# Performance work log

Hardware: AMD Instinct MI355X
Metric: run time of the kernel (lower is better)

Reference implementation:

```python
import jax, jax.numpy as jnp
import numpy as np

EMBED_DIM = 768
HIDDEN_DIM = 768
ASPECT_NUM = 32
BATCH = 256


def setup_inputs() -> dict:
    key = jax.random.key(0)
    k1, k2, k3, k4, k5, k6, k7 = jax.random.split(key, 7)
    s = 0.02
    return {
        "v_X": jax.random.normal(k1, (BATCH, EMBED_DIM), dtype=jnp.float32),
        "v_H": jax.random.normal(k2, (BATCH, HIDDEN_DIM), dtype=jnp.float32),
        "aspect_ids": jax.random.randint(k3, (BATCH,), 0, ASPECT_NUM, dtype=jnp.int64),
        "W1_embs": s * jax.random.normal(k4, (ASPECT_NUM, (EMBED_DIM + HIDDEN_DIM) * HIDDEN_DIM), dtype=jnp.float32),
        "b1_embs": s * jax.random.normal(k5, (ASPECT_NUM, HIDDEN_DIM), dtype=jnp.float32),
        "W2_embs": s * jax.random.normal(k6, (ASPECT_NUM, HIDDEN_DIM * 2), dtype=jnp.float32),
        "b2_embs": s * jax.random.normal(k7, (ASPECT_NUM, 2), dtype=jnp.float32),
    }


def reference(v_X, v_H, aspect_ids, W1_embs, b1_embs, W2_embs, b2_embs):
    batch = v_X.shape[0]
    V = jnp.concatenate([v_X, v_H], axis=-1)  # (B, E+H)
    W1 = W1_embs[aspect_ids].reshape(batch, EMBED_DIM + HIDDEN_DIM, HIDDEN_DIM)
    b1 = b1_embs[aspect_ids]                  # (B, H)
    W2 = W2_embs[aspect_ids].reshape(batch, HIDDEN_DIM, 2)
    b2 = b2_embs[aspect_ids]                  # (B, 2)
    out1 = jax.nn.relu(jnp.einsum('bd,bdh->bh', V, W1) + b1)  # per-sample GEMV
    logits = jnp.einsum('bh,bht->bt', out1, W2) + b2
    return logits
```

## Files before the change

### kernel.cpp

```cpp
#include <hip/hip_runtime.h>
#include <hip/hip_bf16.h>

#define EMBED 768
#define HID 768
#define DTOT 1536
#define NASP 32
#define BATCHN 256
#define CH 16
#define MAXCHUNK 48
#define COLS 32
#define NT2 (HID / COLS)
#define SROWS 192
#define NSTAGE (DTOT / SROWS)
#define VSP 20


__global__ __launch_bounds__(256, 4) void gemv_fused_kernel(
    const float* __restrict__ vX, const float* __restrict__ vH,
    const float* __restrict__ W1, const int* __restrict__ aspect_ids,
    const float* __restrict__ b1, const float* __restrict__ W2,
    float* __restrict__ plog)
{
    __shared__ int wcnt[4][NASP];
    __shared__ int basearr[NASP];
    __shared__ int countsarr[NASP];
    __shared__ int chasp[MAXCHUNK];
    __shared__ int smpall[MAXCHUNK][CH];
    __shared__ int nchunks_s;
    __shared__ __align__(16) float Vs[SROWS * VSP];
    __shared__ __align__(16) float4 redw[8][4][8];

    int t = threadIdx.x;
    int lane = t & 63;
    int wave = t >> 6;
    int myaid = aspect_ids[t];

    unsigned long long mymask = 0ull;
    for (int a = 0; a < NASP; ++a) {
        bool p = (myaid == a);
        unsigned long long m = __ballot(p);
        if (p) mymask = m;
        if (lane == a) wcnt[wave][a] = __popcll(m);
    }
    __syncthreads();
    if (t < NASP) {
        int ctot = wcnt[0][t] + wcnt[1][t] + wcnt[2][t] + wcnt[3][t];
        countsarr[t] = ctot;
        int nc = (ctot + CH - 1) / CH;
        int incl = nc;
        #pragma unroll
        for (int off = 1; off < NASP; off <<= 1) {
            int v = __shfl_up(incl, off, 64);
            if (t >= off) incl += v;
        }
        int base = incl - nc;
        basearr[t] = base;
        for (int j = 0; j < nc; ++j) chasp[base + j] = t;
        if (t == NASP - 1) nchunks_s = incl;
    }
    __syncthreads();
    {
        int pre = 0;
        for (int w = 0; w < wave; ++w) pre += wcnt[w][myaid];
        int r = pre + __popcll(mymask & ((1ull << lane) - 1ull));
        int c = basearr[myaid] + r / CH;
        smpall[c][r % CH] = t;
    }
    __syncthreads();

    int bid = blockIdx.x;
    int chunk = bid / NT2;
    if (chunk >= nchunks_s) return;
    int tile = bid % NT2;

    int aspect = chasp[chunk];
    int cnt = countsarr[aspect] - CH * (chunk - basearr[aspect]);
    if (cnt > CH) cnt = CH;

    int c8 = t & 7;
    int dg = t >> 3;

    const float* wp = W1 + (size_t)aspect * ((size_t)DTOT * HID)
                         + (size_t)dg * HID + tile * COLS + c8 * 4;

    float4 acc[CH];
    #pragma unroll
    for (int s = 0; s < CH; ++s) { acc[s].x = acc[s].y = acc[s].z = acc[s].w = 0.f; }

    for (int st = 0; st < NSTAGE; ++st) {
        int dbase = st * SROWS;
        __syncthreads();
        #pragma unroll
        for (int r = 0; r < 3; ++r) {
            int id = t + r * 256;
            int s = id & (CH - 1);
            int f = id >> 4;
            int smp = (s < cnt) ? smpall[chunk][s] : smpall[chunk][0];
            int d = dbase + f * 4;
            const float* src = (dbase < EMBED)
                ? (vX + (size_t)smp * EMBED + d)
                : (vH + (size_t)smp * HID + (d - EMBED));
            float4 v = *(const float4*)src;
            Vs[(f * 4 + 0) * VSP + s] = v.x;
            Vs[(f * 4 + 1) * VSP + s] = v.y;
            Vs[(f * 4 + 2) * VSP + s] = v.z;
            Vs[(f * 4 + 3) * VSP + s] = v.w;
        }
        __syncthreads();

        #pragma unroll
        for (int kk = 0; kk < SROWS / 32; ++kk) {
            float4 w = *(const float4*)wp;
            wp += 32 * HID;
            const float* vrow = &Vs[(kk * 32 + dg) * VSP];
            float4 va = *(const float4*)(vrow + 0);
            float4 vb = *(const float4*)(vrow + 4);
            float4 vc = *(const float4*)(vrow + 8);
            float4 vd = *(const float4*)(vrow + 12);
            acc[0].x  += va.x * w.x; acc[0].y  += va.x * w.y; acc[0].z  += va.x * w.z; acc[0].w  += va.x * w.w;
            acc[1].x  += va.y * w.x; acc[1].y  += va.y * w.y; acc[1].z  += va.y * w.z; acc[1].w  += va.y * w.w;
            acc[2].x  += va.z * w.x; acc[2].y  += va.z * w.y; acc[2].z  += va.z * w.z; acc[2].w  += va.z * w.w;
            acc[3].x  += va.w * w.x; acc[3].y  += va.w * w.y; acc[3].z  += va.w * w.z; acc[3].w  += va.w * w.w;
            acc[4].x  += vb.x * w.x; acc[4].y  += vb.x * w.y; acc[4].z  += vb.x * w.z; acc[4].w  += vb.x * w.w;
            acc[5].x  += vb.y * w.x; acc[5].y  += vb.y * w.y; acc[5].z  += vb.y * w.z; acc[5].w  += vb.y * w.w;
            acc[6].x  += vb.z * w.x; acc[6].y  += vb.z * w.y; acc[6].z  += vb.z * w.z; acc[6].w  += vb.z * w.w;
            acc[7].x  += vb.w * w.x; acc[7].y  += vb.w * w.y; acc[7].z  += vb.w * w.z; acc[7].w  += vb.w * w.w;
            acc[8].x  += vc.x * w.x; acc[8].y  += vc.x * w.y; acc[8].z  += vc.x * w.z; acc[8].w  += vc.x * w.w;
            acc[9].x  += vc.y * w.x; acc[9].y  += vc.y * w.y; acc[9].z  += vc.y * w.z; acc[9].w  += vc.y * w.w;
            acc[10].x += vc.z * w.x; acc[10].y += vc.z * w.y; acc[10].z += vc.z * w.z; acc[10].w += vc.z * w.w;
            acc[11].x += vc.w * w.x; acc[11].y += vc.w * w.y; acc[11].z += vc.w * w.z; acc[11].w += vc.w * w.w;
            acc[12].x += vd.x * w.x; acc[12].y += vd.x * w.y; acc[12].z += vd.x * w.z; acc[12].w += vd.x * w.w;
            acc[13].x += vd.y * w.x; acc[13].y += vd.y * w.y; acc[13].z += vd.y * w.z; acc[13].w += vd.y * w.w;
            acc[14].x += vd.z * w.x; acc[14].y += vd.z * w.y; acc[14].z += vd.z * w.z; acc[14].w += vd.z * w.w;
            acc[15].x += vd.w * w.x; acc[15].y += vd.w * w.y; acc[15].z += vd.w * w.z; acc[15].w += vd.w * w.w;
        }
    }

    #pragma unroll
    for (int s = 0; s < CH; ++s) {
        float4 v = acc[s];
        v.x += __shfl_down(v.x, 32, 64); v.y += __shfl_down(v.y, 32, 64);
        v.z += __shfl_down(v.z, 32, 64); v.w += __shfl_down(v.w, 32, 64);
        v.x += __shfl_down(v.x, 16, 64); v.y += __shfl_down(v.y, 16, 64);
        v.z += __shfl_down(v.z, 16, 64); v.w += __shfl_down(v.w, 16, 64);
        v.x += __shfl_down(v.x,  8, 64); v.y += __shfl_down(v.y,  8, 64);
        v.z += __shfl_down(v.z,  8, 64); v.w += __shfl_down(v.w,  8, 64);
        acc[s] = v;
    }

    const float* b1p = b1 + (size_t)aspect * HID;
    const float* w2p = W2 + (size_t)aspect * HID * 2;
    #pragma unroll
    for (int rr = 0; rr < 2; ++rr) {
        __syncthreads();
        if (lane < 8) {
            #pragma unroll
            for (int j = 0; j < 8; ++j)
                redw[j][wave][lane] = acc[rr * 8 + j];
        }
        __syncthreads();
        if (wave == 0) {
            int j = t >> 3;
            int c = t & 7;
            int s = rr * 8 + j;
            float4 a0 = redw[j][0][c], a1 = redw[j][1][c];
            float4 a2 = redw[j][2][c], a3 = redw[j][3][c];
            float4 sum;
            sum.x = a0.x + a1.x + a2.x + a3.x;
            sum.y = a0.y + a1.y + a2.y + a3.y;
            sum.z = a0.z + a1.z + a2.z + a3.z;
            sum.w = a0.w + a1.w + a2.w + a3.w;
            int h = tile * COLS + c * 4;
            float p0 = 0.f, p1 = 0.f;
            if (s < cnt) {
                float o;
                o = fmaxf(sum.x + b1p[h + 0], 0.f); p0 += o * w2p[(h + 0) * 2]; p1 += o * w2p[(h + 0) * 2 + 1];
                o = fmaxf(sum.y + b1p[h + 1], 0.f); p0 += o * w2p[(h + 1) * 2]; p1 += o * w2p[(h + 1) * 2 + 1];
                o = fmaxf(sum.z + b1p[h + 2], 0.f); p0 += o * w2p[(h + 2) * 2]; p1 += o * w2p[(h + 2) * 2 + 1];
                o = fmaxf(sum.w + b1p[h + 3], 0.f); p0 += o * w2p[(h + 3) * 2]; p1 += o * w2p[(h + 3) * 2 + 1];
            }
            p0 += __shfl_down(p0, 4, 64); p1 += __shfl_down(p1, 4, 64);
            p0 += __shfl_down(p0, 2, 64); p1 += __shfl_down(p1, 2, 64);
            p0 += __shfl_down(p0, 1, 64); p1 += __shfl_down(p1, 1, 64);
            if (c == 0 && s < cnt) {
                int smp = smpall[chunk][s];
                float2 pv; pv.x = p0; pv.y = p1;
                *(float2*)&plog[((size_t)tile * BATCHN + smp) * 2] = pv;
            }
        }
    }
}

__global__ __launch_bounds__(BATCHN) void combine_kernel(
    const float* __restrict__ plog, const int* __restrict__ aspect_ids,
    const float* __restrict__ b2, float* __restrict__ logits)
{
    int smp = threadIdx.x;
    int a = aspect_ids[smp];
    float p0 = b2[a * 2 + 0], p1 = b2[a * 2 + 1];
    const float2* pl = (const float2*)plog;
    #pragma unroll
    for (int tl = 0; tl < NT2; ++tl) {
        float2 v = pl[(size_t)tl * BATCHN + smp];
        p0 += v.x; p1 += v.y;
    }
    float2 out; out.x = p0; out.y = p1;
    *(float2*)&logits[smp * 2] = out;
}

extern "C" void kernel_launch(void* const* d_in, const int* in_sizes, int n_in,
                              void* d_out, int out_size, void* d_ws, size_t ws_size,
                              hipStream_t stream) {
    const float* vX  = (const float*)d_in[0];
    const float* vH  = (const float*)d_in[1];
    const int*   aid = (const int*)d_in[2];
    const float* W1  = (const float*)d_in[3];
    const float* b1  = (const float*)d_in[4];
    const float* W2  = (const float*)d_in[5];
    const float* b2  = (const float*)d_in[6];
    float* logits = (float*)d_out;

    float* plog = (float*)d_ws;

    gemv_fused_kernel<<<MAXCHUNK * NT2, 256, 0, stream>>>(
        vX, vH, W1, aid, b1, W2, plog);
    combine_kernel<<<1, BATCHN, 0, stream>>>(plog, aid, b2, logits);
}
```

Measured before the change: 48.58 us.

## Widen column tile to 128 and use 512-thread blocks for grouped GEMV

Each block now covers 128 output columns instead of 32 and runs 512 threads, with 32 threads spanning columns and 16 row groups. The gathered V chunk is loaded into shared memory once per 128 columns instead of once per 32, so V traffic and shared-memory staging per block drop. The grid shrinks from 48*24 to 48*6 blocks. The cross-wave reduction now spans 8 waves and needs more rounds. The bigger blocks and fewer of them may lower occupancy and parallelism, and the setup code now places __syncthreads inside divergent branches.

```diff
diff --git a/kernel.cpp b/kernel.cpp
--- a/kernel.cpp
+++ b/kernel.cpp
@@ -8,14 +8,15 @@
 #define BATCHN 256
 #define CH 16
 #define MAXCHUNK 48
-#define COLS 32
-#define NT2 (HID / COLS)
+#define COLS 128
+#define NT (HID / COLS)
 #define SROWS 192
 #define NSTAGE (DTOT / SROWS)
+#define DG 16
 #define VSP 20
 
 
-__global__ __launch_bounds__(256, 4) void gemv_fused_kernel(
+__global__ __launch_bounds__(512, 2) void gemv_fused_kernel(
     const float* __restrict__ vX, const float* __restrict__ vH,
     const float* __restrict__ W1, const int* __restrict__ aspect_ids,
     const float* __restrict__ b1, const float* __restrict__ W2,
@@ -28,60 +29,65 @@
     __shared__ int smpall[MAXCHUNK][CH];
     __shared__ int nchunks_s;
     __shared__ __align__(16) float Vs[SROWS * VSP];
-    __shared__ __align__(16) float4 redw[8][4][8];
+    __shared__ __align__(16) float4 red[4][8][32];
 
     int t = threadIdx.x;
     int lane = t & 63;
     int wave = t >> 6;
-    int myaid = aspect_ids[t];
-
-    unsigned long long mymask = 0ull;
-    for (int a = 0; a < NASP; ++a) {
-        bool p = (myaid == a);
-        unsigned long long m = __ballot(p);
-        if (p) mymask = m;
-        if (lane == a) wcnt[wave][a] = __popcll(m);
+
+    if (t < BATCHN) {
+        int myaid = aspect_ids[t];
+        unsigned long long mymask = 0ull;
+        for (int a = 0; a < NASP; ++a) {
+            bool p = (myaid == a);
+            unsigned long long m = __ballot(p);
+            if (p) mymask = m;
+            if (lane == a) wcnt[wave][a] = __popcll(m);
+        }
+        __syncthreads();
+        if (t < NASP) {
+            int ctot = wcnt[0][t] + wcnt[1][t] + wcnt[2][t] + wcnt[3][t];
+            countsarr[t] = ctot;
+            int nc = (ctot + CH - 1) / CH;
+            int incl = nc;
+            #pragma unroll
+            for (int off = 1; off < NASP; off <<= 1) {
+                int v = __shfl_up(incl, off, 64);
+                if (t >= off) incl += v;
+            }
+            int base = incl - nc;
+            basearr[t] = base;
+            for (int j = 0; j < nc; ++j) chasp[base + j] = t;
+            if (t == NASP - 1) nchunks_s = incl;
+        }
+        __syncthreads();
+        {
+            int pre = 0;
+            for (int w = 0; w < wave; ++w) pre += wcnt[w][myaid];
+            int r = pre + __popcll(mymask & ((1ull << lane) - 1ull));
+            int c = basearr[myaid] + r / CH;
+            smpall[c][r % CH] = t;
+        }
+    } else {
+        __syncthreads();
+        __syncthreads();
     }
     __syncthreads();
-    if (t < NASP) {
-        int ctot = wcnt[0][t] + wcnt[1][t] + wcnt[2][t] + wcnt[3][t];
-        countsarr[t] = ctot;
-        int nc = (ctot + CH - 1) / CH;
-        int incl = nc;
-        #pragma unroll
-        for (int off = 1; off < NASP; off <<= 1) {
-            int v = __shfl_up(incl, off, 64);
-            if (t >= off) incl += v;
-        }
-        int base = incl - nc;
-        basearr[t] = base;
-        for (int j = 0; j < nc; ++j) chasp[base + j] = t;
-        if (t == NASP - 1) nchunks_s = incl;
-    }
-    __syncthreads();
-    {
-        int pre = 0;
-        for (int w = 0; w < wave; ++w) pre += wcnt[w][myaid];
-        int r = pre + __popcll(mymask & ((1ull << lane) - 1ull));
-        int c = basearr[myaid] + r / CH;
-        smpall[c][r % CH] = t;
-    }
-    __syncthreads();
 
     int bid = blockIdx.x;
-    int chunk = bid / NT2;
+    int chunk = bid / NT;
     if (chunk >= nchunks_s) return;
-    int tile = bid % NT2;
+    int tile = bid % NT;
 
     int aspect = chasp[chunk];
     int cnt = countsarr[aspect] - CH * (chunk - basearr[aspect]);
     if (cnt > CH) cnt = CH;
 
-    int c8 = t & 7;
-    int dg = t >> 3;
+    int c32 = t & 31;
+    int dg  = t >> 5;
 
     const float* wp = W1 + (size_t)aspect * ((size_t)DTOT * HID)
-                         + (size_t)dg * HID + tile * COLS + c8 * 4;
+                         + (size_t)dg * HID + tile * COLS + c32 * 4;
 
     float4 acc[CH];
     #pragma unroll
@@ -90,9 +96,8 @@
     for (int st = 0; st < NSTAGE; ++st) {
         int dbase = st * SROWS;
         __syncthreads();
-        #pragma unroll
-        for (int r = 0; r < 3; ++r) {
-            int id = t + r * 256;
+        {
+            int id = t;
             int s = id & (CH - 1);
             int f = id >> 4;
             int smp = (s < cnt) ? smpall[chunk][s] : smpall[chunk][0];
@@ -106,13 +111,28 @@
             Vs[(f * 4 + 2) * VSP + s] = v.z;
             Vs[(f * 4 + 3) * VSP + s] = v.w;
         }
+        if (t < 256) {
+            int id = t + 512;
+            int s = id & (CH - 1);
+            int f = id >> 4;
+            int smp = (s < cnt) ? smpall[chunk][s] : smpall[chunk][0];
+            int d = dbase + f * 4;
+            const float* src = (dbase < EMBED)
+                ? (vX + (size_t)smp * EMBED + d)
+                : (vH + (size_t)smp * HID + (d - EMBED));
+            float4 v = *(const float4*)src;
+            Vs[(f * 4 + 0) * VSP + s] = v.x;
+            Vs[(f * 4 + 1) * VSP + s] = v.y;
+            Vs[(f * 4 + 2) * VSP + s] = v.z;
+            Vs[(f * 4 + 3) * VSP + s] = v.w;
+        }
         __syncthreads();
 
         #pragma unroll
-        for (int kk = 0; kk < SROWS / 32; ++kk) {
+        for (int k = 0; k < SROWS / DG; ++k) {
             float4 w = *(const float4*)wp;
-            wp += 32 * HID;
-            const float* vrow = &Vs[(kk * 32 + dg) * VSP];
+            wp += DG * HID;
+            const float* vrow = &Vs[(k * DG + dg) * VSP];
             float4 va = *(const float4*)(vrow + 0);
             float4 vb = *(const float4*)(vrow + 4);
             float4 vc = *(const float4*)(vrow + 8);
@@ -141,47 +161,44 @@
         float4 v = acc[s];
         v.x += __shfl_down(v.x, 32, 64); v.y += __shfl_down(v.y, 32, 64);
         v.z += __shfl_down(v.z, 32, 64); v.w += __shfl_down(v.w, 32, 64);
-        v.x += __shfl_down(v.x, 16, 64); v.y += __shfl_down(v.y, 16, 64);
-        v.z += __shfl_down(v.z, 16, 64); v.w += __shfl_down(v.w, 16, 64);
-        v.x += __shfl_down(v.x,  8, 64); v.y += __shfl_down(v.y,  8, 64);
-        v.z += __shfl_down(v.z,  8, 64); v.w += __shfl_down(v.w,  8, 64);
         acc[s] = v;
     }
 
     const float* b1p = b1 + (size_t)aspect * HID;
     const float* w2p = W2 + (size_t)aspect * HID * 2;
     #pragma unroll
-    for (int rr = 0; rr < 2; ++rr) {
-        __syncthreads();
-        if (lane < 8) {
+    for (int rr = 0; rr < 4; ++rr) {
+        __syncthreads();
+        if (lane < 32) {
             #pragma unroll
-            for (int j = 0; j < 8; ++j)
-                redw[j][wave][lane] = acc[rr * 8 + j];
-        }
-        __syncthreads();
-        if (wave == 0) {
-            int j = t >> 3;
-            int c = t & 7;
-            int s = rr * 8 + j;
-            float4 a0 = redw[j][0][c], a1 = redw[j][1][c];
-            float4 a2 = redw[j][2][c], a3 = redw[j][3][c];
-            float4 sum;
-            sum.x = a0.x + a1.x + a2.x + a3.x;
-            sum.y = a0.y + a1.y + a2.y + a3.y;
-            sum.z = a0.z + a1.z + a2.z + a3.z;
-            sum.w = a0.w + a1.w + a2.w + a3.w;
-            int h = tile * COLS + c * 4;
+            for (int j = 0; j < 4; ++j)
+                red[j][wave][lane] = acc[rr * 4 + j];
+        }
+        __syncthreads();
+        if (t < 128) {
+            int j = t >> 5;
+            int c = t & 31;
+            int s = rr * 4 + j;
+            float4 sum = red[j][0][c];
+            #pragma unroll
+            for (int g = 1; g < 8; ++g) {
+                float4 o = red[j][g][c];
+                sum.x += o.x; sum.y += o.y; sum.z += o.z; sum.w += o.w;
+            }
             float p0 = 0.f, p1 = 0.f;
             if (s < cnt) {
+                int h = tile * COLS + c * 4;
                 float o;
                 o = fmaxf(sum.x + b1p[h + 0], 0.f); p0 += o * w2p[(h + 0) * 2]; p1 += o * w2p[(h + 0) * 2 + 1];
                 o = fmaxf(sum.y + b1p[h + 1], 0.f); p0 += o * w2p[(h + 1) * 2]; p1 += o * w2p[(h + 1) * 2 + 1];
                 o = fmaxf(sum.z + b1p[h + 2], 0.f); p0 += o * w2p[(h + 2) * 2]; p1 += o * w2p[(h + 2) * 2 + 1];
                 o = fmaxf(sum.w + b1p[h + 3], 0.f); p0 += o * w2p[(h + 3) * 2]; p1 += o * w2p[(h + 3) * 2 + 1];
             }
-            p0 += __shfl_down(p0, 4, 64); p1 += __shfl_down(p1, 4, 64);
-            p0 += __shfl_down(p0, 2, 64); p1 += __shfl_down(p1, 2, 64);
-            p0 += __shfl_down(p0, 1, 64); p1 += __shfl_down(p1, 1, 64);
+            p0 += __shfl_down(p0, 16, 32); p1 += __shfl_down(p1, 16, 32);
+            p0 += __shfl_down(p0,  8, 32); p1 += __shfl_down(p1,  8, 32);
+            p0 += __shfl_down(p0,  4, 32); p1 += __shfl_down(p1,  4, 32);
+            p0 += __shfl_down(p0,  2, 32); p1 += __shfl_down(p1,  2, 32);
+            p0 += __shfl_down(p0,  1, 32); p1 += __shfl_down(p1,  1, 32);
             if (c == 0 && s < cnt) {
                 int smp = smpall[chunk][s];
                 float2 pv; pv.x = p0; pv.y = p1;
@@ -200,7 +217,7 @@
     float p0 = b2[a * 2 + 0], p1 = b2[a * 2 + 1];
     const float2* pl = (const float2*)plog;
     #pragma unroll
-    for (int tl = 0; tl < NT2; ++tl) {
+    for (int tl = 0; tl < NT; ++tl) {
         float2 v = pl[(size_t)tl * BATCHN + smp];
         p0 += v.x; p1 += v.y;
     }
@@ -222,7 +239,7 @@
 
     float* plog = (float*)d_ws;
 
-    gemv_fused_kernel<<<MAXCHUNK * NT2, 256, 0, stream>>>(
+    gemv_fused_kernel<<<MAXCHUNK * NT, 512, 0, stream>>>(
         vX, vH, W1, aid, b1, W2, plog);
     combine_kernel<<<1, BATCHN, 0, stream>>>(plog, aid, b2, logits);
 }
```

After: 43.88 us. 1.11x faster.
